# Performance work log

Hardware: AMD Instinct MI355X
Metric: run time of the kernel (lower is better)

Reference implementation:

```python
import jax, jax.numpy as jnp
import numpy as np

FEAT_DIM = 1024
NUM_HEAD = 8


def setup_inputs() -> dict:
    key = jax.random.key(0)
    ks = jax.random.split(key, 8)
    D = FEAT_DIM
    s = D ** -0.5
    return {
        "motion": jax.random.normal(ks[0], (8, 1024, D), dtype=jnp.float32),
        "scene_feats": jax.random.normal(ks[1], (8, 2048, D), dtype=jnp.float32),
        # nn.Linear weights stored as [in, out] (already transposed for x @ W)
        "Wq": jax.random.normal(ks[2], (D, D), dtype=jnp.float32) * s,
        "bq": jax.random.normal(ks[3], (D,), dtype=jnp.float32) * s,
        "Wkv": jax.random.normal(ks[4], (D, 2 * D), dtype=jnp.float32) * s,
        "bkv": jax.random.normal(ks[5], (2 * D,), dtype=jnp.float32) * s,
        "Wout": jax.random.normal(ks[6], (D, D), dtype=jnp.float32) * s,
        "bout": jax.random.normal(ks[7], (D,), dtype=jnp.float32) * s,
    }


def reference(motion, scene_feats, Wq, bq, Wkv, bkv, Wout, bout):
    bs, L, D = motion.shape
    N = scene_feats.shape[1]
    H = NUM_HEAD
    Dh = D // H

    # q scaled by full feat_dim**-0.5 (as in source, not head_dim)
    q = (motion @ Wq + bq) * (D ** -0.5)
    kv = scene_feats @ Wkv + bkv
    k, v = kv[..., :D], kv[..., D:]

    # Faithful to source: q is viewed as (bs, H, L, Dh) with NO transpose,
    # while k, v use view(bs, N, H, Dh) followed by transpose(1, 2).
    q = q.reshape(bs, H, L, Dh)                      # [bs,H,L,Dh] (layout quirk)
    k = k.reshape(bs, N, H, Dh).transpose(0, 2, 1, 3)  # [bs,H,N,Dh]
    v = v.reshape(bs, N, H, Dh).transpose(0, 2, 1, 3)  # [bs,H,N,Dh]

    att = jnp.einsum("bhld,bhnd->bhln", q, k)        # [bs,H,L,N]
    att = jax.nn.softmax(att, axis=-1)
    out = jnp.einsum("bhln,bhnd->bhld", att, v)      # [bs,H,L,Dh]
    out = out.reshape(bs, L, D)                      # contiguous view, matches torch .view
    return out @ Wout + bout
```

## Files before the change

kernel.cpp:

```cpp
#include <hip/hip_runtime.h>

typedef __attribute__((ext_vector_type(8))) short bf16x8;
typedef __attribute__((ext_vector_type(4))) float f32x4;
typedef __attribute__((ext_vector_type(4))) float f32x4v;
typedef __attribute__((ext_vector_type(4))) int i32x4;

#define MFMA16(a,b,c) __builtin_amdgcn_mfma_f32_16x16x32_bf16((a),(b),(c),0,0,0)

__device__ __forceinline__ short f2bf(float f){
  unsigned u = __builtin_bit_cast(unsigned, f);
  u += 0x7fffu + ((u >> 16) & 1u);
  return (short)(u >> 16);
}

__device__ __forceinline__ void gload16(const void* g, void* l){
  __builtin_amdgcn_global_load_lds((const __attribute__((address_space(1))) unsigned*)g,
                                   (__attribute__((address_space(3))) unsigned*)l,
                                   16, 0, 0);
}

__device__ __forceinline__ int packbf(float a, float b){
  unsigned ua = __builtin_bit_cast(unsigned, a) + 0x7fffu;
  unsigned ub = __builtin_bit_cast(unsigned, b) + 0x7fffu;
  return __builtin_amdgcn_perm(ub, ua, 0x07060302);
}

__global__ __launch_bounds__(256) void k_f2bf(const float* __restrict__ in,
                                              short* __restrict__ out, int n8){
  int i = blockIdx.x * 256 + threadIdx.x;
  if (i >= n8) return;
  f32x4v a = ((const f32x4v*)in)[i*2];
  f32x4v b = ((const f32x4v*)in)[i*2+1];
  bf16x8 o;
  o[0]=f2bf(a[0]); o[1]=f2bf(a[1]); o[2]=f2bf(a[2]); o[3]=f2bf(a[3]);
  o[4]=f2bf(b[0]); o[5]=f2bf(b[1]); o[6]=f2bf(b[2]); o[7]=f2bf(b[3]);
  ((bf16x8*)out)[i] = o;
}

__global__ __launch_bounds__(256) void k_prep_wT(const float* __restrict__ W,
                                                 short* __restrict__ Wt, int K, int N){
  int i = blockIdx.x * 256 + threadIdx.x;
  int total = (K >> 3) * N;
  if (i >= total) return;
  int n  = i % N;
  int k0 = (i / N) << 3;
  bf16x8 o;
#pragma unroll
  for (int j = 0; j < 8; ++j) o[j] = f2bf(W[(size_t)(k0 + j) * N + n]);
  *(bf16x8*)&Wt[(size_t)n * K + k0] = o;
}

template<int MODE>
__global__ __launch_bounds__(256, 4) void k_gemm(
    const short* __restrict__ A, const short* __restrict__ Bt,
    const float* __restrict__ bias, float scale,
    void* __restrict__ out0, void* __restrict__ out1,
    int M, int N, int K)
{
  __shared__ __align__(16) short Alds[3][128 * 32];
  __shared__ __align__(16) short Blds[3][128 * 32];
  const int tid = threadIdx.x;
  const int l = tid & 63, w = tid >> 6;
  const int wr = w >> 1, wc = w & 1;
  const int lr = l & 15, lg = l >> 4;

  const int nx = gridDim.x;
  const int nwg = nx * gridDim.y;
  int flat = blockIdx.y * nx + blockIdx.x;
  int u = (flat & 7) * (nwg >> 3) + (flat >> 3);
  const int m0 = (u / nx) * 128, n0 = (u % nx) * 128;

  const int srow = l >> 2;
  const int scol = 8 * ((l & 3) ^ ((l >> 3) & 3));
  const int acol = 8 * (lg ^ ((lr >> 1) & 3));

  f32x4 acc[4][4];
#pragma unroll
  for (int a = 0; a < 4; ++a)
#pragma unroll
    for (int b = 0; b < 4; ++b) acc[a][b] = (f32x4)(0.0f);

  const int nk = K >> 5;
  auto stage = [&](int kt, int slot){
    int k0 = kt << 5;
#pragma unroll
    for (int i = 0; i < 4; ++i){
      int c = w * 4 + i;
      if (c < 8){
        int m = c * 16 + srow;
        gload16(A + (size_t)(m0 + m) * K + k0 + scol, &Alds[slot][c * 512]);
      } else {
        int n = (c - 8) * 16 + srow;
        gload16(Bt + (size_t)(n0 + n) * K + k0 + scol, &Blds[slot][(c - 8) * 512]);
      }
    }
  };

  stage(0, 0);
  stage(1, 1);
  int rd = 0;
  for (int kt = 0; kt < nk; ++kt){
    asm volatile("s_waitcnt vmcnt(4)" ::: "memory");
    __builtin_amdgcn_s_barrier();
    __builtin_amdgcn_sched_barrier(0);
    int tt = (kt + 2 < nk) ? kt + 2 : nk - 1;
    int tgt = rd + 2; if (tgt >= 3) tgt -= 3;
    stage(tt, tgt);

    bf16x8 af[4], bfv[4];
#pragma unroll
    for (int mi = 0; mi < 4; ++mi){
      int row = wr * 64 + mi * 16 + lr;
      af[mi] = *(const bf16x8*)&Alds[rd][row * 32 + acol];
    }
#pragma unroll
    for (int ni = 0; ni < 4; ++ni){
      int row = wc * 64 + ni * 16 + lr;
      bfv[ni] = *(const bf16x8*)&Blds[rd][row * 32 + acol];
    }
#pragma unroll
    for (int mi = 0; mi < 4; ++mi)
#pragma unroll
      for (int ni = 0; ni < 4; ++ni)
        acc[mi][ni] = MFMA16(af[mi], bfv[ni], acc[mi][ni]);

    if (++rd == 3) rd = 0;
  }
  asm volatile("s_waitcnt vmcnt(0)" ::: "memory");

#pragma unroll
  for (int mi = 0; mi < 4; ++mi)
#pragma unroll
    for (int ni = 0; ni < 4; ++ni){
      int col = n0 + wc * 64 + ni * 16 + lr;
      float bv = bias[col];
#pragma unroll
      for (int r = 0; r < 4; ++r){
        int row = m0 + wr * 64 + mi * 16 + lg * 4 + r;
        float v = acc[mi][ni][r] + bv;
        if (MODE == 0){
          v *= scale;
          int b = row >> 10, lp = row & 1023;
          int h = lp >> 7;
          int lq = ((lp & 127) << 3) | (col >> 7);
          int dh = col & 127;
          ((short*)out0)[(((size_t)(b * 8 + h)) * 1024 + lq) * 128 + dh] = f2bf(v);
        } else {
          ((float*)out0)[(size_t)row * N + col] = v;
        }
      }
    }
}

__global__ __launch_bounds__(512, 2) void k_gemmKV(
    const short* __restrict__ A, const short* __restrict__ Bt,
    const float* __restrict__ bias,
    short* __restrict__ out0, short* __restrict__ out1)
{
  __shared__ __align__(16) short As[3][256 * 32];
  __shared__ __align__(16) short Bs[3][256 * 32];
  const int tid = threadIdx.x;
  const int l = tid & 63, w = tid >> 6;
  const int lr = l & 15, lg = l >> 4;
  const int wm = w >> 2, wn = w & 3;

  int flat = blockIdx.y * 8 + blockIdx.x;
  int u = (flat & 7) * 64 + (flat >> 3);
  const int m0 = (u >> 3) * 256, n0 = (u & 7) * 256;

  const int srow = l >> 2;
  const int scol = 8 * ((l & 3) ^ ((l >> 3) & 3));
  const int acol = 8 * (lg ^ ((lr >> 1) & 3));

  f32x4 acc[8][4];
#pragma unroll
  for (int a = 0; a < 8; ++a)
#pragma unroll
    for (int b = 0; b < 4; ++b) acc[a][b] = (f32x4)(0.0f);

  auto stage = [&](int kt, int slot){
    int k0 = kt << 5;
#pragma unroll
    for (int i = 0; i < 4; ++i){
      int c = w * 4 + i;
      if (c < 16){
        int m = c * 16 + srow;
        gload16(A + (size_t)(m0 + m) * 1024 + k0 + scol, &As[slot][c * 512]);
      } else {
        int n = (c - 16) * 16 + srow;
        gload16(Bt + (size_t)(n0 + n) * 1024 + k0 + scol, &Bs[slot][(c - 16) * 512]);
      }
    }
  };

  stage(0, 0);
  stage(1, 1);
  int rd = 0;
  for (int kt = 0; kt < 32; ++kt){
    asm volatile("s_waitcnt vmcnt(4)" ::: "memory");
    __builtin_amdgcn_s_barrier();
    __builtin_amdgcn_sched_barrier(0);
    int tt = (kt + 2 < 32) ? kt + 2 : 31;
    int tgt = rd + 2; if (tgt >= 3) tgt -= 3;
    stage(tt, tgt);

    bf16x8 af[8], bfv[4];
#pragma unroll
    for (int mi = 0; mi < 8; ++mi){
      int row = wm * 128 + mi * 16 + lr;
      af[mi] = *(const bf16x8*)&As[rd][row * 32 + acol];
    }
#pragma unroll
    for (int ni = 0; ni < 4; ++ni){
      int row = wn * 64 + ni * 16 + lr;
      bfv[ni] = *(const bf16x8*)&Bs[rd][row * 32 + acol];
    }
    __builtin_amdgcn_s_setprio(1);
#pragma unroll
    for (int mi = 0; mi < 8; ++mi)
#pragma unroll
      for (int ni = 0; ni < 4; ++ni)
        acc[mi][ni] = MFMA16(af[mi], bfv[ni], acc[mi][ni]);
    __builtin_amdgcn_s_setprio(0);

    if (++rd == 3) rd = 0;
  }
  asm volatile("s_waitcnt vmcnt(0)" ::: "memory");

#pragma unroll
  for (int mi = 0; mi < 8; ++mi)
#pragma unroll
    for (int ni = 0; ni < 4; ++ni){
      int col = n0 + wn * 64 + ni * 16 + lr;
      float bv = bias[col];
#pragma unroll
      for (int r = 0; r < 4; ++r){
        int row = m0 + wm * 128 + mi * 16 + lg * 4 + r;
        float v = acc[mi][ni][r] + bv;
        int b = row >> 11, nn = row & 2047;
        if (col < 1024){
          int h = col >> 7, dh = col & 127;
          out0[(((size_t)(b * 8 + h)) * 2048 + nn) * 128 + dh] = f2bf(v);
        } else {
          int c2 = col - 1024, h = c2 >> 7, dh = c2 & 127;
          out1[(((size_t)(b * 8 + h)) * 128 + dh) * 2048 + nn] = f2bf(v);
        }
      }
    }
}

__global__ __launch_bounds__(256, 2) void k_attn(
    const short* __restrict__ Q, const short* __restrict__ K,
    const short* __restrict__ Vt, short* __restrict__ O)
{
  __shared__ __align__(16) short Klds[2][64 * 128];
  __shared__ __align__(16) short Vlds[2][128 * 64];
  const int tid = threadIdx.x;
  const int l = tid & 63, w = tid >> 6;
  const int lr = l & 15, lg = l >> 4;

  int flat = blockIdx.y * 8 + blockIdx.x;
  int xcd = flat & 7, idx = flat >> 3;
  int bh = xcd * 8 + (idx >> 3);
  int q0 = (idx & 7) * 128;
  const int qbase = q0 + w * 32;

  const short* Qb = Q  + (size_t)bh * 1024 * 128;
  const short* Kb = K  + (size_t)bh * 2048 * 128;
  const short* Vb = Vt + (size_t)bh * 128 * 2048;

  bf16x8 qf[2][4];
#pragma unroll
  for (int mi = 0; mi < 2; ++mi)
#pragma unroll
    for (int kc = 0; kc < 4; ++kc)
      qf[mi][kc] = *(const bf16x8*)&Qb[(size_t)(qbase + mi * 16 + lr) * 128 + kc * 32 + lg * 8];

  f32x4 acc[2][8];
#pragma unroll
  for (int mi = 0; mi < 2; ++mi)
#pragma unroll
    for (int d = 0; d < 8; ++d) acc[mi][d] = (f32x4)(0.0f);
  float mrun[2] = {-3e38f, -3e38f}, lsum[2] = {0.f, 0.f};

  const int addrA = 4 * ((l & 15) + 32 * ((l >> 4) & 1));
  const int addrB = addrA + 64;
  const bool hi = (l >= 32);

  auto stageK = [&](int t, int buf){
    int kv0 = t * 64;
#pragma unroll
    for (int i = 0; i < 4; ++i){
      int c = w * 4 + i;
      int row = 4 * c + (l >> 4);
      int col = ((l & 15) * 8) ^ ((row & 7) * 8);
      gload16(Kb + (size_t)(kv0 + row) * 128 + col, &Klds[buf][c * 512]);
    }
  };
  auto stageV = [&](int t, int buf){
    int kv0 = t * 64;
#pragma unroll
    for (int i = 0; i < 4; ++i){
      int c = w * 4 + i;
      int dh = 8 * c + (l >> 3);
      int col = ((l & 7) * 8) ^ (((l >> 3) & 7) * 8);
      gload16(Vb + (size_t)dh * 2048 + kv0 + col, &Vlds[buf][c * 512]);
    }
  };

  stageK(0, 0); stageV(0, 0);
  __syncthreads();
  int cur = 0;
  const int swz = (lr & 7) * 8;

  for (int t = 0; t < 32; ++t){
    if (t + 1 < 32){ stageK(t + 1, cur ^ 1); stageV(t + 1, cur ^ 1); }
    const short* Kl = &Klds[cur][0];
    const short* Vl = &Vlds[cur][0];

    f32x4 s[2][4];
    __builtin_amdgcn_s_setprio(1);
#pragma unroll
    for (int nt = 0; nt < 4; ++nt){
      f32x4 s0 = (f32x4)(0.0f), s1 = (f32x4)(0.0f);
#pragma unroll
      for (int kc = 0; kc < 4; ++kc){
        bf16x8 kf = *(const bf16x8*)&Kl[(nt * 16 + lr) * 128 + ((kc * 32 + lg * 8) ^ swz)];
        s0 = MFMA16(kf, qf[0][kc], s0);
        s1 = MFMA16(kf, qf[1][kc], s1);
      }
      s[0][nt] = s0; s[1][nt] = s1;
    }
    __builtin_amdgcn_s_setprio(0);

    float mloc[2];
    int ok = 1;
#pragma unroll
    for (int mi = 0; mi < 2; ++mi){
      float v = fmaxf(fmaxf(fmaxf(s[mi][0][0], s[mi][0][1]), fmaxf(s[mi][0][2], s[mi][0][3])),
                      fmaxf(fmaxf(s[mi][1][0], s[mi][1][1]), fmaxf(s[mi][1][2], s[mi][1][3])));
      v = fmaxf(v, fmaxf(fmaxf(fmaxf(s[mi][2][0], s[mi][2][1]), fmaxf(s[mi][2][2], s[mi][2][3])),
                         fmaxf(fmaxf(s[mi][3][0], s[mi][3][1]), fmaxf(s[mi][3][2], s[mi][3][3]))));
      mloc[mi] = v;
      ok &= (v <= mrun[mi] + 8.0f) ? 1 : 0;
    }
    if (!__all(ok)){
#pragma unroll
      for (int mi = 0; mi < 2; ++mi){
        float v = mloc[mi];
        v = fmaxf(v, __shfl_xor(v, 16));
        v = fmaxf(v, __shfl_xor(v, 32));
        float mnew = fmaxf(mrun[mi], v);
        float sc = exp2f(mrun[mi] - mnew);
        mrun[mi] = mnew;
        lsum[mi] *= sc;
#pragma unroll
        for (int r = 0; r < 4; ++r){
          float scr = __shfl(sc, 20 * lg + r);
#pragma unroll
          for (int d = 0; d < 8; ++d) acc[mi][d][r] *= scr;
        }
      }
    }

    int pk[2][4][2];
#pragma unroll
    for (int mi = 0; mi < 2; ++mi){
      float ls = 0.f;
#pragma unroll
      for (int nt = 0; nt < 4; ++nt){
        float p0 = exp2f(s[mi][nt][0] - mrun[mi]);
        float p1 = exp2f(s[mi][nt][1] - mrun[mi]);
        float p2 = exp2f(s[mi][nt][2] - mrun[mi]);
        float p3 = exp2f(s[mi][nt][3] - mrun[mi]);
        ls += (p0 + p1) + (p2 + p3);
        pk[mi][nt][0] = packbf(p0, p1);
        pk[mi][nt][1] = packbf(p2, p3);
      }
      lsum[mi] += ls;
    }

    bf16x8 pa[2][2];
#pragma unroll
    for (int mi = 0; mi < 2; ++mi)
#pragma unroll
      for (int kc = 0; kc < 2; ++kc){
        i32x4 dw;
#pragma unroll
        for (int av = 0; av < 2; ++av){
          int addr = av ? addrB : addrA;
#pragma unroll
          for (int jj = 0; jj < 2; ++jj){
            int t0 = __builtin_amdgcn_ds_bpermute(addr, pk[mi][2 * kc][jj]);
            int t1 = __builtin_amdgcn_ds_bpermute(addr, pk[mi][2 * kc + 1][jj]);
            dw[av * 2 + jj] = hi ? t1 : t0;
          }
        }
        pa[mi][kc] = __builtin_bit_cast(bf16x8, dw);
      }

    __builtin_amdgcn_s_setprio(1);
#pragma unroll
    for (int d = 0; d < 8; ++d)
#pragma unroll
      for (int kc = 0; kc < 2; ++kc){
        bf16x8 vf = *(const bf16x8*)&Vl[(d * 16 + lr) * 64 + ((kc * 32 + lg * 8) ^ swz)];
        acc[0][d] = MFMA16(pa[0][kc], vf, acc[0][d]);
        acc[1][d] = MFMA16(pa[1][kc], vf, acc[1][d]);
      }
    __builtin_amdgcn_s_setprio(0);

    __syncthreads();
    cur ^= 1;
  }

  const int b = bh >> 3, h = bh & 7;
#pragma unroll
  for (int mi = 0; mi < 2; ++mi){
    float ls = lsum[mi];
    ls += __shfl_xor(ls, 16);
    ls += __shfl_xor(ls, 32);
    float inv = 1.0f / ls;
#pragma unroll
    for (int r = 0; r < 4; ++r){
      float invr = __shfl(inv, 20 * lg + r);
      int grow = qbase + mi * 16 + lg * 4 + r;
      size_t base = ((size_t)b * 1024 + (size_t)h * 128 + (grow >> 3)) * 1024
                  + (size_t)(grow & 7) * 128;
#pragma unroll
      for (int d = 0; d < 8; ++d)
        O[base + d * 16 + lr] = f2bf(acc[mi][d][r] * invr);
    }
  }
}

extern "C" void kernel_launch(void* const* d_in, const int* in_sizes, int n_in,
                              void* d_out, int out_size, void* d_ws, size_t ws_size,
                              hipStream_t stream){
  const float* motion = (const float*)d_in[0];
  const float* scene  = (const float*)d_in[1];
  const float* Wq     = (const float*)d_in[2];
  const float* bq     = (const float*)d_in[3];
  const float* Wkv    = (const float*)d_in[4];
  const float* bkv    = (const float*)d_in[5];
  const float* Wout   = (const float*)d_in[6];
  const float* bout   = (const float*)d_in[7];
  float* out = (float*)d_out;

  char* ws = (char*)d_ws;
  const size_t MB = 1024 * 1024;
  short* WqT   = (short*)(ws + 0);
  short* WkvT  = (short*)(ws + 2  * MB);
  short* WoutT = (short*)(ws + 6  * MB);
  short* mA    = (short*)(ws + 8  * MB);
  short* sA    = (short*)(ws + 24 * MB);
  short* Qb    = (short*)(ws + 56 * MB);
  short* Kb    = (short*)(ws + 72 * MB);
  short* Vtb   = (short*)(ws + 104* MB);
  short* attnO = mA;

  const float qscale = 0.03125f * 1.44269504088896341f;

  k_prep_wT<<<dim3(512),  256, 0, stream>>>(Wq,   WqT,   1024, 1024);
  k_prep_wT<<<dim3(1024), 256, 0, stream>>>(Wkv,  WkvT,  1024, 2048);
  k_prep_wT<<<dim3(512),  256, 0, stream>>>(Wout, WoutT, 1024, 1024);
  k_f2bf<<<dim3(4096), 256, 0, stream>>>(motion, mA, 1024 * 1024);
  k_f2bf<<<dim3(8192), 256, 0, stream>>>(scene,  sA, 2 * 1024 * 1024);

  k_gemm<0><<<dim3(8, 64), 256, 0, stream>>>(mA, WqT, bq, qscale, Qb, nullptr, 8192, 1024, 1024);
  k_gemmKV<<<dim3(8, 64), 512, 0, stream>>>(sA, WkvT, bkv, Kb, Vtb);
  k_attn<<<dim3(8, 64), 256, 0, stream>>>(Qb, Kb, Vtb, attnO);
  k_gemm<2><<<dim3(8, 64), 256, 0, stream>>>(attnO, WoutT, bout, 1.0f, out, nullptr, 8192, 1024, 1024);
}
```

Baseline: 302.9 us.

## Merge Q and KV projection GEMMs into one grouped 256x256-tile launch

Replaces the separate Q projection GEMM (128-tile kernel) and KV projection GEMM with a single grouped kernel over 640 tiles: 512 KV tiles plus 128 Q tiles, all using the 256x256 tile shape. This removes one launch and the tail of the smaller Q GEMM, and moves Q onto the larger tile for better reuse. The pipeline also drops from triple to double buffering with a full vmcnt(0) wait each iteration. That reduces LDS use but exposes more load latency.

```diff
diff --git a/kernel.cpp b/kernel.cpp
--- a/kernel.cpp
+++ b/kernel.cpp
@@ -48,6 +48,114 @@
 #pragma unroll
   for (int j = 0; j < 8; ++j) o[j] = f2bf(W[(size_t)(k0 + j) * N + n]);
   *(bf16x8*)&Wt[(size_t)n * K + k0] = o;
+}
+
+__global__ __launch_bounds__(512, 2) void k_mm256(
+    const short* __restrict__ sA, const short* __restrict__ mA,
+    const short* __restrict__ WkvT, const short* __restrict__ WqT,
+    const float* __restrict__ bkv, const float* __restrict__ bq,
+    float qscale,
+    short* __restrict__ Kb, short* __restrict__ Vtb, short* __restrict__ Qb)
+{
+  __shared__ __align__(16) short As[2][256 * 32];
+  __shared__ __align__(16) short Bs[2][256 * 32];
+  const int tid = threadIdx.x;
+  const int l = tid & 63, w = tid >> 6;
+  const int lr = l & 15, lg = l >> 4;
+  const int wm = w >> 2, wn = w & 3;
+
+  int flat = blockIdx.y * 8 + blockIdx.x;
+  int u = (flat & 7) * 80 + (flat >> 3);
+  const bool kv = (u < 512);
+  int m0, n0;
+  const short *Ap, *Bp;
+  const float* biasp;
+  if (kv){ m0 = (u >> 3) * 256;            n0 = (u & 7) * 256;  Ap = sA; Bp = WkvT; biasp = bkv; }
+  else   { int u2 = u - 512;
+           m0 = (u2 >> 2) * 256;           n0 = (u2 & 3) * 256; Ap = mA; Bp = WqT;  biasp = bq;  }
+
+  const int srow = l >> 2;
+  const int scol = 8 * ((l & 3) ^ ((l >> 3) & 3));
+  const int acol = 8 * (lg ^ ((lr >> 1) & 3));
+
+  f32x4 acc[8][4];
+#pragma unroll
+  for (int a = 0; a < 8; ++a)
+#pragma unroll
+    for (int b = 0; b < 4; ++b) acc[a][b] = (f32x4)(0.0f);
+
+  auto stage = [&](int kt, int slot){
+    int k0 = kt << 5;
+#pragma unroll
+    for (int i = 0; i < 4; ++i){
+      int c = w * 4 + i;
+      if (c < 16){
+        int m = c * 16 + srow;
+        gload16(Ap + (size_t)(m0 + m) * 1024 + k0 + scol, &As[slot][c * 512]);
+      } else {
+        int n = (c - 16) * 16 + srow;
+        gload16(Bp + (size_t)(n0 + n) * 1024 + k0 + scol, &Bs[slot][(c - 16) * 512]);
+      }
+    }
+  };
+
+  stage(0, 0);
+  for (int kt = 0; kt < 32; ++kt){
+    asm volatile("s_waitcnt vmcnt(0)" ::: "memory");
+    __builtin_amdgcn_s_barrier();
+    __builtin_amdgcn_sched_barrier(0);
+    if (kt + 1 < 32) stage(kt + 1, (kt + 1) & 1);
+    const int rd = kt & 1;
+
+    bf16x8 af[8], bfv[4];
+#pragma unroll
+    for (int mi = 0; mi < 8; ++mi){
+      int row = wm * 128 + mi * 16 + lr;
+      af[mi] = *(const bf16x8*)&As[rd][row * 32 + acol];
+    }
+#pragma unroll
+    for (int ni = 0; ni < 4; ++ni){
+      int row = wn * 64 + ni * 16 + lr;
+      bfv[ni] = *(const bf16x8*)&Bs[rd][row * 32 + acol];
+    }
+    __builtin_amdgcn_s_setprio(1);
+#pragma unroll
+    for (int mi = 0; mi < 8; ++mi)
+#pragma unroll
+      for (int ni = 0; ni < 4; ++ni)
+        acc[mi][ni] = MFMA16(af[mi], bfv[ni], acc[mi][ni]);
+    __builtin_amdgcn_s_setprio(0);
+  }
+
+#pragma unroll
+  for (int mi = 0; mi < 8; ++mi)
+#pragma unroll
+    for (int ni = 0; ni < 4; ++ni){
+      int col = n0 + wn * 64 + ni * 16 + lr;
+      float bv = biasp[col];
+#pragma unroll
+      for (int r = 0; r < 4; ++r){
+        int row = m0 + wm * 128 + mi * 16 + lg * 4 + r;
+        float v = acc[mi][ni][r] + bv;
+        if (kv){
+          int b = row >> 11, nn = row & 2047;
+          if (col < 1024){
+            int h = col >> 7, dh = col & 127;
+            Kb[(((size_t)(b * 8 + h)) * 2048 + nn) * 128 + dh] = f2bf(v);
+          } else {
+            int c2 = col - 1024, h = c2 >> 7, dh = c2 & 127;
+            Vtb[(((size_t)(b * 8 + h)) * 128 + dh) * 2048 + nn] = f2bf(v);
+          }
+        } else {
+          v *= qscale;
+          int b = row >> 10, lp = row & 1023;
+          int h = lp >> 7;
+          int lq = ((lp & 127) << 3) | (col >> 7);
+          int dh = col & 127;
+          Qb[(((size_t)(b * 8 + h)) * 1024 + lq) * 128 + dh] = f2bf(v);
+        }
+      }
+    }
 }
 
 template<int MODE>
@@ -152,103 +260,6 @@
     }
 }
 
-__global__ __launch_bounds__(512, 2) void k_gemmKV(
-    const short* __restrict__ A, const short* __restrict__ Bt,
-    const float* __restrict__ bias,
-    short* __restrict__ out0, short* __restrict__ out1)
-{
-  __shared__ __align__(16) short As[3][256 * 32];
-  __shared__ __align__(16) short Bs[3][256 * 32];
-  const int tid = threadIdx.x;
-  const int l = tid & 63, w = tid >> 6;
-  const int lr = l & 15, lg = l >> 4;
-  const int wm = w >> 2, wn = w & 3;
-
-  int flat = blockIdx.y * 8 + blockIdx.x;
-  int u = (flat & 7) * 64 + (flat >> 3);
-  const int m0 = (u >> 3) * 256, n0 = (u & 7) * 256;
-
-  const int srow = l >> 2;
-  const int scol = 8 * ((l & 3) ^ ((l >> 3) & 3));
-  const int acol = 8 * (lg ^ ((lr >> 1) & 3));
-
-  f32x4 acc[8][4];
-#pragma unroll
-  for (int a = 0; a < 8; ++a)
-#pragma unroll
-    for (int b = 0; b < 4; ++b) acc[a][b] = (f32x4)(0.0f);
-
-  auto stage = [&](int kt, int slot){
-    int k0 = kt << 5;
-#pragma unroll
-    for (int i = 0; i < 4; ++i){
-      int c = w * 4 + i;
-      if (c < 16){
-        int m = c * 16 + srow;
-        gload16(A + (size_t)(m0 + m) * 1024 + k0 + scol, &As[slot][c * 512]);
-      } else {
-        int n = (c - 16) * 16 + srow;
-        gload16(Bt + (size_t)(n0 + n) * 1024 + k0 + scol, &Bs[slot][(c - 16) * 512]);
-      }
-    }
-  };
-
-  stage(0, 0);
-  stage(1, 1);
-  int rd = 0;
-  for (int kt = 0; kt < 32; ++kt){
-    asm volatile("s_waitcnt vmcnt(4)" ::: "memory");
-    __builtin_amdgcn_s_barrier();
-    __builtin_amdgcn_sched_barrier(0);
-    int tt = (kt + 2 < 32) ? kt + 2 : 31;
-    int tgt = rd + 2; if (tgt >= 3) tgt -= 3;
-    stage(tt, tgt);
-
-    bf16x8 af[8], bfv[4];
-#pragma unroll
-    for (int mi = 0; mi < 8; ++mi){
-      int row = wm * 128 + mi * 16 + lr;
-      af[mi] = *(const bf16x8*)&As[rd][row * 32 + acol];
-    }
-#pragma unroll
-    for (int ni = 0; ni < 4; ++ni){
-      int row = wn * 64 + ni * 16 + lr;
-      bfv[ni] = *(const bf16x8*)&Bs[rd][row * 32 + acol];
-    }
-    __builtin_amdgcn_s_setprio(1);
-#pragma unroll
-    for (int mi = 0; mi < 8; ++mi)
-#pragma unroll
-      for (int ni = 0; ni < 4; ++ni)
-        acc[mi][ni] = MFMA16(af[mi], bfv[ni], acc[mi][ni]);
-    __builtin_amdgcn_s_setprio(0);
-
-    if (++rd == 3) rd = 0;
-  }
-  asm volatile("s_waitcnt vmcnt(0)" ::: "memory");
-
-#pragma unroll
-  for (int mi = 0; mi < 8; ++mi)
-#pragma unroll
-    for (int ni = 0; ni < 4; ++ni){
-      int col = n0 + wn * 64 + ni * 16 + lr;
-      float bv = bias[col];
-#pragma unroll
-      for (int r = 0; r < 4; ++r){
-        int row = m0 + wm * 128 + mi * 16 + lg * 4 + r;
-        float v = acc[mi][ni][r] + bv;
-        int b = row >> 11, nn = row & 2047;
-        if (col < 1024){
-          int h = col >> 7, dh = col & 127;
-          out0[(((size_t)(b * 8 + h)) * 2048 + nn) * 128 + dh] = f2bf(v);
-        } else {
-          int c2 = col - 1024, h = c2 >> 7, dh = c2 & 127;
-          out1[(((size_t)(b * 8 + h)) * 128 + dh) * 2048 + nn] = f2bf(v);
-        }
-      }
-    }
-}
-
 __global__ __launch_bounds__(256, 2) void k_attn(
     const short* __restrict__ Q, const short* __restrict__ K,
     const short* __restrict__ Vt, short* __restrict__ O)
@@ -467,8 +478,7 @@
   k_f2bf<<<dim3(4096), 256, 0, stream>>>(motion, mA, 1024 * 1024);
   k_f2bf<<<dim3(8192), 256, 0, stream>>>(scene,  sA, 2 * 1024 * 1024);
 
-  k_gemm<0><<<dim3(8, 64), 256, 0, stream>>>(mA, WqT, bq, qscale, Qb, nullptr, 8192, 1024, 1024);
-  k_gemmKV<<<dim3(8, 64), 512, 0, stream>>>(sA, WkvT, bkv, Kb, Vtb);
+  k_mm256<<<dim3(8, 80), 512, 0, stream>>>(sA, mA, WkvT, WqT, bkv, bq, qscale, Kb, Vtb, Qb);
   k_attn<<<dim3(8, 64), 256, 0, stream>>>(Qb, Kb, Vtb, attnO);
   k_gemm<2><<<dim3(8, 64), 256, 0, stream>>>(attnO, WoutT, bout, 1.0f, out, nullptr, 8192, 1024, 1024);
 }
```

After: 318.8 us. 5.3% more time.
